# Kernel optimization log

Measured on AMD Instinct MI355X. Metric: run time of the kernel, lower is better.

Reference implementation:

```python
import jax, jax.numpy as jnp
import numpy as np

S, B, C, H, M = 384, 8, 1024, 16, 1536
CC = C // H


def setup_inputs() -> dict:
    key = jax.random.key(0)
    ks = jax.random.split(key, 8)
    x = jax.random.normal(ks[0], (S, B, C), dtype=jnp.float32)
    pe = jax.random.normal(ks[1], (S, B, C), dtype=jnp.float32)
    memory_k = jax.random.normal(ks[2], (M, B, H, CC), dtype=jnp.float32)
    memory_v = jax.random.normal(ks[3], (M, B, H, CC), dtype=jnp.float32)
    w_qkv = jax.random.normal(ks[4], (C, 3 * C), dtype=jnp.float32) * 0.02
    b_qkv = jnp.zeros((3 * C,), dtype=jnp.float32)
    w_out = jax.random.normal(ks[5], (C, C), dtype=jnp.float32) * 0.02
    b_out = jnp.zeros((C,), dtype=jnp.float32)
    terminal = jnp.zeros((B,), dtype=bool)
    # causal mask over the new tokens: True = masked (future positions)
    content_mask = jnp.broadcast_to(
        (jnp.arange(S)[None, :] > jnp.arange(S)[:, None])[:, :, None], (S, S, B))
    padding_mask = jnp.zeros((S, B), dtype=bool)  # True = padded
    memory_length = jax.random.randint(ks[6], (B,), 0, M, dtype=jnp.int32)
    return dict(x=x, positional_encoding=pe, memory_k=memory_k, memory_v=memory_v,
                w_qkv=w_qkv, b_qkv=b_qkv, w_out=w_out, b_out=b_out,
                terminal=terminal, content_mask=content_mask,
                padding_mask=padding_mask, memory_length=memory_length)


def reference(x, positional_encoding, memory_k, memory_v, w_qkv, b_qkv,
              w_out, b_out, terminal, content_mask, padding_mask, memory_length):
    s, b, c = x.shape
    # qkv projection
    qkv = (x + positional_encoding) @ w_qkv + b_qkv          # [s,b,3c]
    q, k, v = jnp.split(qkv, 3, axis=-1)
    q = q.reshape(s, b, H, CC)
    k = k.reshape(s, b, H, CC)
    v = v.reshape(s, b, H, CC)
    # clear_memory(terminal): zero lengths for terminal episodes
    mem_len = jnp.where(terminal, 0, memory_length)          # [b]
    # ragged memory concat expressed with fixed capacity M + padding mask
    k_full = jnp.concatenate([memory_k, k], axis=0)          # [M+s,b,H,CC]
    v_full = jnp.concatenate([memory_v, v], axis=0)
    mem_pad = jnp.arange(M)[:, None] >= mem_len[None, :]     # [M,b] True=masked
    kv_pad = jnp.concatenate([mem_pad, padding_mask], axis=0)  # [M+s,b]
    mem_content = jnp.zeros((s, M, b), dtype=bool)           # memory visible to all queries
    full_content = jnp.concatenate([mem_content, content_mask], axis=1)  # [s,M+s,b]
    mask = full_content | kv_pad[None, :, :]                 # [s,M+s,b]
    # attention
    scores = jnp.einsum('sbhc,tbhc->stbh', q, k_full) * (1.0 / np.sqrt(CC))
    scores = jnp.where(mask[:, :, :, None], jnp.float32(-1e9), scores)
    p = jax.nn.softmax(scores, axis=1)                       # [s,M+s,b,h]
    out = jnp.einsum('stbh,tbhc->sbhc', p, v_full).reshape(s, b, c)
    return out @ w_out + b_out
```

## Files before the change

### kernel.cpp

```cpp
#include <hip/hip_runtime.h>
#include <math.h>

#define S_DIM 384
#define B_DIM 8
#define C_DIM 1024
#define H_DIM 16
#define M_DIM 1536
#define CC_DIM 64
#define ROWS  (S_DIM * B_DIM)
#define N3C   (3 * C_DIM)
#define CHUNK 6
#define MAXS  5

typedef unsigned short u16;
typedef short bf8v  __attribute__((ext_vector_type(8)));
typedef short bf4v  __attribute__((ext_vector_type(4)));
typedef u16   us8   __attribute__((ext_vector_type(8)));
typedef u16   us4   __attribute__((ext_vector_type(4)));
typedef float f4v   __attribute__((ext_vector_type(4)));

__device__ __forceinline__ u16 f2bf(float f) {
    unsigned u = __float_as_uint(f);
    u += 0x7fffu + ((u >> 16) & 1u);
    return (u16)(u >> 16);
}
__device__ __forceinline__ float bf2f(u16 v) {
    return __uint_as_float(((unsigned)v) << 16);
}
#if __has_builtin(__builtin_amdgcn_exp2f)
#define EX2(x) __builtin_amdgcn_exp2f(x)
#else
#define EX2(x) __expf((x) * 0.69314718056f)
#endif
#define QSCALE (0.125f * 1.44269504f)

__device__ __forceinline__ f4v mfma16x16x16bf16(bf4v a, bf4v b, f4v c) {
#if __has_builtin(__builtin_amdgcn_mfma_f32_16x16x16bf16_1k)
    return __builtin_amdgcn_mfma_f32_16x16x16bf16_1k(a, b, c, 0, 0, 0);
#else
    return c;
#endif
}

__device__ __forceinline__ void gload16(const u16* g, u16* l) {
    __builtin_amdgcn_global_load_lds(
        (const __attribute__((address_space(1))) void*)g,
        (__attribute__((address_space(3))) void*)l, 16, 0, 0);
}

__device__ __forceinline__ void tr_direct(const float* __restrict__ in,
                                          u16* __restrict__ out,
                                          int R, int Cc, int r0, int c0, int tid) {
    const int c4 = c0 + (tid & 15) * 4;
    const int rq = r0 + (tid >> 4) * 4;
    float4 L[4];
    #pragma unroll
    for (int k = 0; k < 4; k++)
        L[k] = *(const float4*)(in + (size_t)(rq + k) * Cc + c4);
    #pragma unroll
    for (int j = 0; j < 4; j++) {
        us4 o;
        o[0] = f2bf(((const float*)&L[0])[j]);
        o[1] = f2bf(((const float*)&L[1])[j]);
        o[2] = f2bf(((const float*)&L[2])[j]);
        o[3] = f2bf(((const float*)&L[3])[j]);
        *(us4*)(out + (size_t)(c4 + j) * R + rq) = o;
    }
}

__global__ __launch_bounds__(256) void prep_all(
    const float* __restrict__ x, const float* __restrict__ pe, u16* __restrict__ Abf,
    const float* __restrict__ wqkv, u16* __restrict__ Wqkvt,
    const float* __restrict__ wout, u16* __restrict__ Woutt,
    const float* __restrict__ mk, u16* __restrict__ mk_bf,
    const float* __restrict__ mv, u16* __restrict__ mv_t)
{
    const int bid = blockIdx.x, tid = threadIdx.x;

    if (bid < 768) {
        size_t i0 = (size_t)bid * 4096 + tid * 16;
        float4 xv[4], pv[4];
        #pragma unroll
        for (int j = 0; j < 4; j++) {
            xv[j] = *(const float4*)(x + i0 + j * 4);
            pv[j] = *(const float4*)(pe + i0 + j * 4);
        }
        #pragma unroll
        for (int h8 = 0; h8 < 2; h8++) {
            us8 o;
            #pragma unroll
            for (int j = 0; j < 2; j++) {
                float4 a = xv[h8 * 2 + j], p = pv[h8 * 2 + j];
                o[j * 4 + 0] = f2bf(a.x + p.x);
                o[j * 4 + 1] = f2bf(a.y + p.y);
                o[j * 4 + 2] = f2bf(a.z + p.z);
                o[j * 4 + 3] = f2bf(a.w + p.w);
            }
            *(us8*)(Abf + i0 + h8 * 8) = o;
        }
    } else if (bid < 1536) {
        int b2 = bid - 768;
        tr_direct(wqkv, Wqkvt, C_DIM, N3C, (b2 / 48) * 64, (b2 % 48) * 64, tid);
    } else if (bid < 1792) {
        int b3 = bid - 1536;
        tr_direct(wout, Woutt, C_DIM, C_DIM, (b3 / 16) * 64, (b3 % 16) * 64, tid);
    } else if (bid < 4864) {
        size_t i0 = (size_t)(bid - 1792) * 4096 + tid * 16;
        float4 v[4];
        #pragma unroll
        for (int j = 0; j < 4; j++)
            v[j] = *(const float4*)(mk + i0 + j * 4);
        #pragma unroll
        for (int h8 = 0; h8 < 2; h8++) {
            us8 o;
            #pragma unroll
            for (int j = 0; j < 2; j++) {
                float4 a = v[h8 * 2 + j];
                o[j * 4 + 0] = f2bf(a.x);
                o[j * 4 + 1] = f2bf(a.y);
                o[j * 4 + 2] = f2bf(a.z);
                o[j * 4 + 3] = f2bf(a.w);
            }
            *(us8*)(mk_bf + i0 + h8 * 8) = o;
        }
    } else {
        int b5 = bid - 4864;
        int bh = b5 & 127;
        int t0 = (b5 >> 7) * 64;
        const int cc4 = (tid & 15) * 4;
        const int t = t0 + (tid >> 4) * 4;
        float4 L[4];
        #pragma unroll
        for (int k = 0; k < 4; k++)
            L[k] = *(const float4*)(mv + ((size_t)(t + k) * 128 + bh) * 64 + cc4);
        #pragma unroll
        for (int j = 0; j < 4; j++) {
            us4 o;
            o[0] = f2bf(((const float*)&L[0])[j]);
            o[1] = f2bf(((const float*)&L[1])[j]);
            o[2] = f2bf(((const float*)&L[2])[j]);
            o[3] = f2bf(((const float*)&L[3])[j]);
            *(us4*)(mv_t + ((size_t)bh * 64 + cc4 + j) * M_DIM + t) = o;
        }
    }
}

__global__ __launch_bounds__(256) void qkv_gemm(
    const u16* __restrict__ Abf, const u16* __restrict__ Wt,
    const float* __restrict__ bias,
    u16* __restrict__ Qw, u16* __restrict__ Kw, u16* __restrict__ Vwt)
{
    __shared__ u16 smem[128 * 64 + 64 * 64];
    u16* As = smem;
    u16* Bs = smem + 128 * 64;
    u16* Cs = smem;

    const int tid = threadIdx.x;
    const int lane = tid & 63, w = tid >> 6;
    const int lr = lane & 15, quad = lane >> 4;
    const int wm = w >> 1, wn = w & 1;
    const int row0 = blockIdx.y * 128, col0 = blockIdx.x * 64;

    f4v acc[4][2];
    #pragma unroll
    for (int i = 0; i < 4; i++)
        #pragma unroll
        for (int j = 0; j < 2; j++)
            acc[i][j] = (f4v){0.f, 0.f, 0.f, 0.f};

    for (int k0 = 0; k0 < C_DIM; k0 += 64) {
        __syncthreads();
        #pragma unroll
        for (int j = 0; j < 4; j++) {
            int idx = j * 256 + tid;
            int r = idx >> 3, c = (idx & 7) ^ (r & 7);
            gload16(&Abf[(size_t)(row0 + r) * C_DIM + k0 + c * 8], &As[idx * 8]);
        }
        #pragma unroll
        for (int j = 0; j < 2; j++) {
            int idx = j * 256 + tid;
            int r = idx >> 3, c = (idx & 7) ^ (r & 7);
            gload16(&Wt[(size_t)(col0 + r) * C_DIM + k0 + c * 8], &Bs[idx * 8]);
        }
        __syncthreads();
        #pragma unroll
        for (int kh = 0; kh < 2; kh++) {
            bf8v a[4], b[2];
            #pragma unroll
            for (int mi = 0; mi < 4; mi++) {
                int row = wm * 64 + mi * 16 + lr;
                int p = (kh * 4 + quad) ^ (lr & 7);
                a[mi] = *(const bf8v*)&As[row * 64 + p * 8];
            }
            #pragma unroll
            for (int nj = 0; nj < 2; nj++) {
                int row = wn * 32 + nj * 16 + lr;
                int p = (kh * 4 + quad) ^ (lr & 7);
                b[nj] = *(const bf8v*)&Bs[row * 64 + p * 8];
            }
            #pragma unroll
            for (int mi = 0; mi < 4; mi++)
                #pragma unroll
                for (int nj = 0; nj < 2; nj++)
                    acc[mi][nj] = __builtin_amdgcn_mfma_f32_16x16x32_bf16(a[mi], b[nj], acc[mi][nj], 0, 0, 0);
        }
    }

    const int which = col0 >> 10;
    const int h = (col0 >> 6) & 15;
    const float qs = (which == 0) ? QSCALE : 1.0f;

    __syncthreads();
    #pragma unroll
    for (int nj = 0; nj < 2; nj++) {
        int col = col0 + wn * 32 + nj * 16 + lr;
        float bv = bias[col];
        #pragma unroll
        for (int mi = 0; mi < 4; mi++)
            #pragma unroll
            for (int reg = 0; reg < 4; reg++)
                Cs[(wm * 64 + mi * 16 + quad * 4 + reg) * 72 + wn * 32 + nj * 16 + lr] =
                    f2bf((acc[mi][nj][reg] + bv) * qs);
    }
    __syncthreads();

    if (which != 2) {
        u16* dstbuf = (which == 0) ? Qw : Kw;
        int r = tid >> 1, half = tid & 1;
        int rg = row0 + r, s = rg >> 3, bb = rg & 7;
        u16* drow = dstbuf + ((size_t)(bb * 16 + h) * S_DIM + s) * 64 + half * 32;
        #pragma unroll
        for (int i = 0; i < 4; i++)
            *(us8*)(drow + i * 8) = *(const us8*)&Cs[r * 72 + half * 32 + i * 8];
    } else {
        int cc = tid & 63, w4 = tid >> 6;
        int s0 = row0 >> 3;
        #pragma unroll
        for (int pb = 0; pb < 2; pb++) {
            int bb = w4 * 2 + pb;
            us8 v0, v1;
            #pragma unroll
            for (int sl = 0; sl < 8; sl++) {
                v0[sl] = Cs[(sl * 8 + bb) * 72 + cc];
                v1[sl] = Cs[((sl + 8) * 8 + bb) * 72 + cc];
            }
            u16* dr = Vwt + ((size_t)(bb * 16 + h) * 64 + cc) * S_DIM + s0;
            *(us8*)dr = v0;
            *(us8*)(dr + 8) = v1;
        }
    }
}

__global__ __launch_bounds__(256) void attn_split(
    const u16* __restrict__ Qw, const u16* __restrict__ Kw,
    const u16* __restrict__ mk_bf, const u16* __restrict__ Vwt,
    const u16* __restrict__ mv_t, const unsigned char* __restrict__ terminal,
    const int* __restrict__ mem_len, u16* __restrict__ Op, float* __restrict__ ml)
{
    __shared__ u16 Ks[64 * 64];
    __shared__ u16 Vs[64 * 64];

    const int tid = threadIdx.x;
    const int lane = tid & 63, w = tid >> 6;
    const int lr = lane & 15, quad = lane >> 4, q8 = quad * 8;
    const int bid = blockIdx.x;
    const int j = bid % MAXS;
    const int g = bid / MAXS;
    const int b = g & 7, h = (g >> 3) & 15, sc = g >> 7;
    const int bh = b * 16 + h, sq0 = sc * 64;
    const int L = terminal[b] ? 0 : mem_len[b];
    const int memChunks = (L + 63) >> 6;
    const int total = memChunks + sc + 1;
    const int lo = j * CHUNK;
    const int hi = (lo + CHUNK < total) ? lo + CHUNK : total;
    if (lo >= total) return;

    const int qrow = sq0 + w * 16 + lr;

    const u16* qbase = Qw + ((size_t)bh * S_DIM + sq0 + w * 16 + lr) * 64;
    bf8v qf0 = *(const bf8v*)&qbase[q8];
    bf8v qf1 = *(const bf8v*)&qbase[32 + q8];

    f4v O[4];
    #pragma unroll
    for (int nj = 0; nj < 4; nj++) O[nj] = (f4v){0.f, 0.f, 0.f, 0.f};
    float m_i = -1e30f, l_i = 0.0f;

    const f4v zero = (f4v){0.f, 0.f, 0.f, 0.f};

    for (int ch = lo; ch < hi; ch++) {
        const bool isMem = (ch < memChunks);
        const int tloc = isMem ? ch * 64 : (ch - memChunks) * 64;
        const u16* kb; size_t kstr;
        if (isMem) { kb = mk_bf + ((size_t)tloc * 128 + bh) * 64; kstr = 128 * 64; }
        else       { kb = Kw + ((size_t)bh * S_DIM + tloc) * 64; kstr = 64; }
        const u16* vb; size_t vstr;
        if (isMem) { vb = mv_t + (size_t)bh * 64 * M_DIM + tloc; vstr = M_DIM; }
        else       { vb = Vwt + (size_t)bh * 64 * S_DIM + tloc; vstr = S_DIM; }

        __syncthreads();
        #pragma unroll
        for (int jj = 0; jj < 2; jj++) {
            int idx = jj * 256 + tid;
            int r = idx >> 3, c = (idx & 7) ^ (r & 7);
            gload16(kb + (size_t)r * kstr + c * 8, &Ks[idx * 8]);
        }
        #pragma unroll
        for (int jj = 0; jj < 2; jj++) {
            int idx = jj * 256 + tid;
            int cc = idx >> 3, c = (idx & 7) ^ (cc & 7);
            gload16(vb + (size_t)cc * vstr + c * 8, &Vs[idx * 8]);
        }
        __syncthreads();

        f4v sv[4];
        #pragma unroll
        for (int tt = 0; tt < 4; tt++) {
            int row = tt * 16 + lr;
            int p0 = quad ^ (lr & 7), p1 = (4 + quad) ^ (lr & 7);
            bf8v k0 = *(const bf8v*)&Ks[row * 64 + p0 * 8];
            bf8v k1 = *(const bf8v*)&Ks[row * 64 + p1 * 8];
            sv[tt] = __builtin_amdgcn_mfma_f32_16x16x32_bf16(k0, qf0, zero, 0, 0, 0);
            sv[tt] = __builtin_amdgcn_mfma_f32_16x16x32_bf16(k1, qf1, sv[tt], 0, 0, 0);
        }

        if (isMem) {
            if (tloc + 64 > L) {
                #pragma unroll
                for (int tt = 0; tt < 4; tt++)
                    #pragma unroll
                    for (int reg = 0; reg < 4; reg++) {
                        int t = tloc + tt * 16 + quad * 4 + reg;
                        if (t >= L) sv[tt][reg] = -1e30f;
                    }
            }
        } else {
            if (tloc + 63 > sq0 + w * 16) {
                #pragma unroll
                for (int tt = 0; tt < 4; tt++)
                    #pragma unroll
                    for (int reg = 0; reg < 4; reg++) {
                        int t = tloc + tt * 16 + quad * 4 + reg;
                        if (t > qrow) sv[tt][reg] = -1e30f;
                    }
            }
        }

        float rowmax = fmaxf(fmaxf(sv[0][0], sv[0][1]), fmaxf(sv[0][2], sv[0][3]));
        #pragma unroll
        for (int tt = 1; tt < 4; tt++)
            rowmax = fmaxf(rowmax, fmaxf(fmaxf(sv[tt][0], sv[tt][1]),
                                         fmaxf(sv[tt][2], sv[tt][3])));
        rowmax = fmaxf(rowmax, __shfl_xor(rowmax, 16));
        rowmax = fmaxf(rowmax, __shfl_xor(rowmax, 32));
        float mnew = fmaxf(m_i, rowmax);
        float alpha = EX2(m_i - mnew);
        m_i = mnew;
        float sum = 0.0f;
        bf4v pf[4];
        #pragma unroll
        for (int tt = 0; tt < 4; tt++) {
            #pragma unroll
            for (int reg = 0; reg < 4; reg++) {
                float p = EX2(sv[tt][reg] - mnew);
                sum += p;
                pf[tt][reg] = (short)f2bf(p);
            }
        }
        sum += __shfl_xor(sum, 16);
        sum += __shfl_xor(sum, 32);
        l_i = l_i * alpha + sum;

        float alphaR[4];
        #pragma unroll
        for (int reg = 0; reg < 4; reg++)
            alphaR[reg] = __shfl(alpha, quad * 4 + reg);
        #pragma unroll
        for (int nj = 0; nj < 4; nj++)
            #pragma unroll
            for (int reg = 0; reg < 4; reg++)
                O[nj][reg] *= alphaR[reg];

        #pragma unroll
        for (int tt = 0; tt < 4; tt++) {
            #pragma unroll
            for (int nj = 0; nj < 4; nj++) {
                int cc = nj * 16 + lr;
                int c = (tt * 2 + (quad >> 1)) ^ (lr & 7);
                bf4v vf = *(const bf4v*)&Vs[cc * 64 + c * 8 + (quad & 1) * 4];
                O[nj] = mfma16x16x16bf16(pf[tt], vf, O[nj]);
            }
        }
    }

    const size_t pbase = (size_t)(g * MAXS + j) * 64;
    if (quad == 0) {
        int row = w * 16 + lr;
        float2 mlv = {m_i, l_i};
        *(float2*)&ml[(pbase + row) * 2] = mlv;
    }
    #pragma unroll
    for (int reg = 0; reg < 4; reg++) {
        int row = w * 16 + quad * 4 + reg;
        #pragma unroll
        for (int nj = 0; nj < 4; nj++)
            Op[(pbase + row) * 64 + nj * 16 + lr] = f2bf(O[nj][reg]);
    }
}

__global__ __launch_bounds__(256) void attn_combine(
    const unsigned char* __restrict__ terminal, const int* __restrict__ mem_len,
    const u16* __restrict__ Op, const float* __restrict__ ml, u16* __restrict__ Obf)
{
    const int g = blockIdx.x;
    const int b = g & 7, h = (g >> 3) & 15, sc = g >> 7;
    const int tid = threadIdx.x;
    const int row = tid >> 2, c0 = (tid & 3) * 16;

    const int L = terminal[b] ? 0 : mem_len[b];
    const int total = ((L + 63) >> 6) + sc + 1;
    const int nsp = (total + CHUNK - 1) / CHUNK;

    float m[MAXS], lv[MAXS];
    #pragma unroll
    for (int j = 0; j < MAXS; j++) {
        if (j < nsp) {
            size_t base = (size_t)(g * MAXS + j) * 64 + row;
            m[j]  = ml[base * 2];
            lv[j] = ml[base * 2 + 1];
        } else { m[j] = -1e30f; lv[j] = 0.0f; }
    }
    float mstar = m[0];
    #pragma unroll
    for (int j = 1; j < MAXS; j++) mstar = fmaxf(mstar, m[j]);
    float sc_j[MAXS], l = 0.0f;
    #pragma unroll
    for (int j = 0; j < MAXS; j++) {
        sc_j[j] = (j < nsp) ? EX2(m[j] - mstar) : 0.0f;
        l += sc_j[j] * lv[j];
    }
    float inv = 1.0f / l;

    float o[16];
    #pragma unroll
    for (int c = 0; c < 16; c++) o[c] = 0.0f;
    for (int j = 0; j < nsp; j++) {
        const u16* src = &Op[((size_t)(g * MAXS + j) * 64 + row) * 64 + c0];
        us8 v0 = *(const us8*)src;
        us8 v1 = *(const us8*)(src + 8);
        #pragma unroll
        for (int c = 0; c < 8; c++) {
            o[c]     += sc_j[j] * bf2f(v0[c]);
            o[c + 8] += sc_j[j] * bf2f(v1[c]);
        }
    }
    int s = sc * 64 + row;
    size_t dst = ((size_t)s * 8 + b) * C_DIM + h * 64 + c0;
    us8 w0, w1;
    #pragma unroll
    for (int c = 0; c < 8; c++) {
        w0[c] = f2bf(o[c] * inv);
        w1[c] = f2bf(o[c + 8] * inv);
    }
    *(us8*)&Obf[dst] = w0;
    *(us8*)&Obf[dst + 8] = w1;
}

__global__ __launch_bounds__(256) void proj_gemm(
    const u16* __restrict__ Abf, const u16* __restrict__ Wt,
    const float* __restrict__ bias, float* __restrict__ out)
{
    __shared__ u16 As[64 * 64];
    __shared__ u16 Bs[64 * 64];
    const int tid = threadIdx.x;
    const int lane = tid & 63, w = tid >> 6;
    const int lr = lane & 15, quad = lane >> 4;
    const int row0 = blockIdx.y * 64, col0 = blockIdx.x * 64;

    f4v acc[4];
    #pragma unroll
    for (int i = 0; i < 4; i++) acc[i] = (f4v){0.f, 0.f, 0.f, 0.f};

    for (int k0 = 0; k0 < C_DIM; k0 += 64) {
        __syncthreads();
        #pragma unroll
        for (int j = 0; j < 2; j++) {
            int idx = j * 256 + tid;
            int r = idx >> 3, c = (idx & 7) ^ (r & 7);
            gload16(&Abf[(size_t)(row0 + r) * C_DIM + k0 + c * 8], &As[idx * 8]);
            gload16(&Wt[(size_t)(col0 + r) * C_DIM + k0 + c * 8], &Bs[idx * 8]);
        }
        __syncthreads();
        #pragma unroll
        for (int kh = 0; kh < 2; kh++) {
            int p = (kh * 4 + quad) ^ (lr & 7);
            bf8v a = *(const bf8v*)&As[(w * 16 + lr) * 64 + p * 8];
            #pragma unroll
            for (int nj = 0; nj < 4; nj++) {
                bf8v bfr = *(const bf8v*)&Bs[(nj * 16 + lr) * 64 + p * 8];
                acc[nj] = __builtin_amdgcn_mfma_f32_16x16x32_bf16(a, bfr, acc[nj], 0, 0, 0);
            }
        }
    }

    #pragma unroll
    for (int nj = 0; nj < 4; nj++) {
        int col = col0 + nj * 16 + lr;
        float bv = bias[col];
        #pragma unroll
        for (int reg = 0; reg < 4; reg++) {
            int rg = row0 + w * 16 + quad * 4 + reg;
            out[(size_t)rg * C_DIM + col] = acc[nj][reg] + bv;
        }
    }
}

extern "C" void kernel_launch(void* const* d_in, const int* in_sizes, int n_in,
                              void* d_out, int out_size, void* d_ws, size_t ws_size,
                              hipStream_t stream) {
    const float* x    = (const float*)d_in[0];
    const float* pe   = (const float*)d_in[1];
    const float* mk   = (const float*)d_in[2];
    const float* mv   = (const float*)d_in[3];
    const float* wqkv = (const float*)d_in[4];
    const float* bqkv = (const float*)d_in[5];
    const float* wout = (const float*)d_in[6];
    const float* bout = (const float*)d_in[7];
    const unsigned char* term = (const unsigned char*)d_in[8];
    const int* mem_len = (const int*)d_in[11];

    char* ws = (char*)d_ws;
    u16* Abf   = (u16*)(ws + 0);
    u16* Obf   = (u16*)(ws + 0);
    u16* Wqkvt = (u16*)(ws + 6291456);
    float* ml  = (float*)(ws + 6291456);
    u16* Woutt = (u16*)(ws + 12582912);
    u16* mk_bf = (u16*)(ws + 14680064);
    u16* mv_t  = (u16*)(ws + 39845888);
    u16* Qw    = (u16*)(ws + 65011712);
    u16* Kw    = (u16*)(ws + 71303168);
    u16* Vwt   = (u16*)(ws + 77594624);
    u16* Op    = (u16*)(ws + 83886080);

    float* out = (float*)d_out;

    prep_all<<<7936, 256, 0, stream>>>(x, pe, Abf, wqkv, Wqkvt, wout, Woutt,
                                       mk, mk_bf, mv, mv_t);

    qkv_gemm<<<dim3(N3C / 64, ROWS / 128), 256, 0, stream>>>(
        Abf, Wqkvt, bqkv, Qw, Kw, Vwt);

    attn_split<<<B_DIM * H_DIM * (S_DIM / 64) * MAXS, 256, 0, stream>>>(
        Qw, Kw, mk_bf, Vwt, mv_t, term, mem_len, Op, ml);

    attn_combine<<<B_DIM * H_DIM * (S_DIM / 64), 256, 0, stream>>>(
        term, mem_len, Op, ml, Obf);

    proj_gemm<<<dim3(C_DIM / 64, ROWS / 64), 256, 0, stream>>>(
        Obf, Woutt, bout, out);
}
```

Baseline: 285.5 us.

## Skip converting unused memory rows in prep, widen transposes, raise MFMA priority

The prep kernel now reads terminal and memory_length and skips bf16 conversion and transposition of memory K/V rows beyond each batch's valid length (rounded up to 64). This removes most of the memory-tensor traffic, which dominates prep. It also widens the weight and V transposes to 8 rows per thread so stores are 16 bytes, and reorders the block ranges. The attention kernel additionally wraps its MFMA loops in s_setprio hints. Skipped rows are left stale, which is safe only if the attention kernel never reads tiles at or beyond the rounded length.

New measurement: 274.9 us. 1.04x faster.

```diff
diff --git a/kernel.cpp b/kernel.cpp
--- a/kernel.cpp
+++ b/kernel.cpp
@@ -48,23 +48,22 @@
         (__attribute__((address_space(3))) void*)l, 16, 0, 0);
 }
 
-__device__ __forceinline__ void tr_direct(const float* __restrict__ in,
-                                          u16* __restrict__ out,
-                                          int R, int Cc, int r0, int c0, int tid) {
+__device__ __forceinline__ void tr_direct8(const float* __restrict__ in,
+                                           u16* __restrict__ out,
+                                           int R, int Cc, int r0, int c0, int tid) {
     const int c4 = c0 + (tid & 15) * 4;
-    const int rq = r0 + (tid >> 4) * 4;
-    float4 L[4];
-    #pragma unroll
-    for (int k = 0; k < 4; k++)
+    const int rq = r0 + (tid >> 4) * 8;
+    float4 L[8];
+    #pragma unroll
+    for (int k = 0; k < 8; k++)
         L[k] = *(const float4*)(in + (size_t)(rq + k) * Cc + c4);
     #pragma unroll
     for (int j = 0; j < 4; j++) {
-        us4 o;
-        o[0] = f2bf(((const float*)&L[0])[j]);
-        o[1] = f2bf(((const float*)&L[1])[j]);
-        o[2] = f2bf(((const float*)&L[2])[j]);
-        o[3] = f2bf(((const float*)&L[3])[j]);
-        *(us4*)(out + (size_t)(c4 + j) * R + rq) = o;
+        us8 o;
+        #pragma unroll
+        for (int k = 0; k < 8; k++)
+            o[k] = f2bf(((const float*)&L[k])[j]);
+        *(us8*)(out + (size_t)(c4 + j) * R + rq) = o;
     }
 }
 
@@ -73,12 +72,54 @@
     const float* __restrict__ wqkv, u16* __restrict__ Wqkvt,
     const float* __restrict__ wout, u16* __restrict__ Woutt,
     const float* __restrict__ mk, u16* __restrict__ mk_bf,
-    const float* __restrict__ mv, u16* __restrict__ mv_t)
+    const float* __restrict__ mv, u16* __restrict__ mv_t,
+    const unsigned char* __restrict__ terminal, const int* __restrict__ mem_len)
 {
     const int bid = blockIdx.x, tid = threadIdx.x;
 
-    if (bid < 768) {
-        size_t i0 = (size_t)bid * 4096 + tid * 16;
+    if (bid < 1536) {
+        const int bh = bid & 127, tg = bid >> 7;
+        const int t0 = tg * 128;
+        const int b = bh >> 4;
+        const int L = terminal[b] ? 0 : mem_len[b];
+        const int Lc = ((L + 63) >> 6) << 6;
+        if (t0 >= Lc) return;
+        const int cc4 = (tid & 15) * 4;
+        const int tq = t0 + (tid >> 4) * 8;
+        float4 Lv[8];
+        #pragma unroll
+        for (int k = 0; k < 8; k++)
+            Lv[k] = *(const float4*)(mv + ((size_t)(tq + k) * 128 + bh) * 64 + cc4);
+        #pragma unroll
+        for (int j = 0; j < 4; j++) {
+            us8 o;
+            #pragma unroll
+            for (int k = 0; k < 8; k++)
+                o[k] = f2bf(((const float*)&Lv[k])[j]);
+            *(us8*)(mv_t + ((size_t)bh * 64 + cc4 + j) * M_DIM + tq) = o;
+        }
+    } else if (bid < 4608) {
+        const int b6 = bid - 1536;
+        const int b = b6 & 7, t0 = (b6 >> 3) * 4;
+        const int L = terminal[b] ? 0 : mem_len[b];
+        const int Lc = ((L + 63) >> 6) << 6;
+        if (t0 >= Lc) return;
+        const int r = t0 + (tid >> 6);
+        const size_t rb = (size_t)r * 8192 + (size_t)b * 1024;
+        const int cw = (tid & 63) * 4;
+        float4 v[4];
+        #pragma unroll
+        for (int j = 0; j < 4; j++)
+            v[j] = *(const float4*)(mk + rb + cw + j * 256);
+        #pragma unroll
+        for (int j = 0; j < 4; j++) {
+            us4 o;
+            o[0] = f2bf(v[j].x); o[1] = f2bf(v[j].y);
+            o[2] = f2bf(v[j].z); o[3] = f2bf(v[j].w);
+            *(us4*)(mk_bf + rb + cw + j * 256) = o;
+        }
+    } else if (bid < 5376) {
+        size_t i0 = (size_t)(bid - 4608) * 4096 + tid * 16;
         float4 xv[4], pv[4];
         #pragma unroll
         for (int j = 0; j < 4; j++) {
@@ -98,50 +139,12 @@
             }
             *(us8*)(Abf + i0 + h8 * 8) = o;
         }
-    } else if (bid < 1536) {
-        int b2 = bid - 768;
-        tr_direct(wqkv, Wqkvt, C_DIM, N3C, (b2 / 48) * 64, (b2 % 48) * 64, tid);
-    } else if (bid < 1792) {
-        int b3 = bid - 1536;
-        tr_direct(wout, Woutt, C_DIM, C_DIM, (b3 / 16) * 64, (b3 % 16) * 64, tid);
-    } else if (bid < 4864) {
-        size_t i0 = (size_t)(bid - 1792) * 4096 + tid * 16;
-        float4 v[4];
-        #pragma unroll
-        for (int j = 0; j < 4; j++)
-            v[j] = *(const float4*)(mk + i0 + j * 4);
-        #pragma unroll
-        for (int h8 = 0; h8 < 2; h8++) {
-            us8 o;
-            #pragma unroll
-            for (int j = 0; j < 2; j++) {
-                float4 a = v[h8 * 2 + j];
-                o[j * 4 + 0] = f2bf(a.x);
-                o[j * 4 + 1] = f2bf(a.y);
-                o[j * 4 + 2] = f2bf(a.z);
-                o[j * 4 + 3] = f2bf(a.w);
-            }
-            *(us8*)(mk_bf + i0 + h8 * 8) = o;
-        }
+    } else if (bid < 5760) {
+        const int b2 = bid - 5376;
+        tr_direct8(wqkv, Wqkvt, C_DIM, N3C, (b2 / 48) * 128, (b2 % 48) * 64, tid);
     } else {
-        int b5 = bid - 4864;
-        int bh = b5 & 127;
-        int t0 = (b5 >> 7) * 64;
-        const int cc4 = (tid & 15) * 4;
-        const int t = t0 + (tid >> 4) * 4;
-        float4 L[4];
-        #pragma unroll
-        for (int k = 0; k < 4; k++)
-            L[k] = *(const float4*)(mv + ((size_t)(t + k) * 128 + bh) * 64 + cc4);
-        #pragma unroll
-        for (int j = 0; j < 4; j++) {
-            us4 o;
-            o[0] = f2bf(((const float*)&L[0])[j]);
-            o[1] = f2bf(((const float*)&L[1])[j]);
-            o[2] = f2bf(((const float*)&L[2])[j]);
-            o[3] = f2bf(((const float*)&L[3])[j]);
-            *(us4*)(mv_t + ((size_t)bh * 64 + cc4 + j) * M_DIM + t) = o;
-        }
+        const int b3 = bid - 5760;
+        tr_direct8(wout, Woutt, C_DIM, C_DIM, (b3 / 16) * 128, (b3 % 16) * 64, tid);
     }
 }
 
@@ -314,6 +317,7 @@
         __syncthreads();
 
         f4v sv[4];
+        __builtin_amdgcn_s_setprio(1);
         #pragma unroll
         for (int tt = 0; tt < 4; tt++) {
             int row = tt * 16 + lr;
@@ -323,6 +327,7 @@
             sv[tt] = __builtin_amdgcn_mfma_f32_16x16x32_bf16(k0, qf0, zero, 0, 0, 0);
             sv[tt] = __builtin_amdgcn_mfma_f32_16x16x32_bf16(k1, qf1, sv[tt], 0, 0, 0);
         }
+        __builtin_amdgcn_s_setprio(0);
 
         if (isMem) {
             if (tloc + 64 > L) {
@@ -381,6 +386,7 @@
             for (int reg = 0; reg < 4; reg++)
                 O[nj][reg] *= alphaR[reg];
 
+        __builtin_amdgcn_s_setprio(1);
         #pragma unroll
         for (int tt = 0; tt < 4; tt++) {
             #pragma unroll
@@ -391,6 +397,7 @@
                 O[nj] = mfma16x16x16bf16(pf[tt], vf, O[nj]);
             }
         }
+        __builtin_amdgcn_s_setprio(0);
     }
 
     const size_t pbase = (size_t)(g * MAXS + j) * 64;
@@ -544,8 +551,8 @@
 
     float* out = (float*)d_out;
 
-    prep_all<<<7936, 256, 0, stream>>>(x, pe, Abf, wqkv, Wqkvt, wout, Woutt,
-                                       mk, mk_bf, mv, mv_t);
+    prep_all<<<5888, 256, 0, stream>>>(x, pe, Abf, wqkv, Wqkvt, wout, Woutt,
+                                       mk, mk_bf, mv, mv_t, term, mem_len);
 
     qkv_gemm<<<dim3(N3C / 64, ROWS / 128), 256, 0, stream>>>(
         Abf, Wqkvt, bqkv, Qw, Kw, Vwt);
```
